# Kernel optimization log

Measured on AMD Instinct MI355X. Metric: run time of the kernel, lower is better.

## Reference

```python
import jax, jax.numpy as jnp
import numpy as np

T, G, L_UH, NZ = 512, 4096, 15, 1e-5

PHY_NAMES = ['ddf_min','ddf_plus','Kcum','Kf','exp_fe','Tbf','Ccum','SWI','Tbm','fcmin','fcmin_plus','vadose_max_level','hmets_alpha','vic_beta','hbv_beta','quickflow_k','quickflow_n','mmax','lamb','baseflow_k','baseflow_n','ET_efficiency','coef_vadose2phreatic','coef_phreatic']
BOUNDS = {'ddf_min':(0.,20.),'ddf_plus':(0.,20.),'Kcum':(.01,.2),'Kf':(0.,5.),'exp_fe':(0.,1.),'Tbf':(-5.,2.),'Ccum':(.005,.05),'SWI':(0.,.4),'Tbm':(-2.,3.),'fcmin':(0.,.1),'fcmin_plus':(.01,.25),'vadose_max_level':(.001,500.),'hmets_alpha':(0.,1.),'vic_beta':(.1,3.),'hbv_beta':(.5,3.),'quickflow_k':(-5.,-2.),'quickflow_n':(.5,2.),'mmax':(0.,100.),'lamb':(5.,10.),'baseflow_k':(-5.,-1.),'baseflow_n':(.5,2.),'ET_efficiency':(0.,3.),'coef_vadose2phreatic':(1e-5,.02),'coef_phreatic':(1e-5,.01)}

def setup_inputs():
    key = jax.random.key(0)
    k1, k2, k3, k4 = jax.random.split(key, 4)
    prcp = jax.random.uniform(k1, (T, G)) * 20.0   # mm/day
    tmean = jax.random.uniform(k2, (T, G)) * 40.0 - 15.0  # deg C, mixed rain/snow
    pet = jax.random.uniform(k3, (T, G)) * 6.0
    x = jnp.stack([prcp, tmean, pet], axis=-1).astype(jnp.float32)
    parameters = jax.random.normal(k4, (T, G, 39), dtype=jnp.float32)
    return {'x': x, 'parameters': parameters}

def _descale(v, lo, hi):
    return lo + v * (hi - lo)

def _unpack(parameters):
    # static params: last time step (dynamic_params=[], dy_drop=0 -> staPar path)
    last = parameters[-1, :, :35]
    p = {n: _descale(jax.nn.sigmoid(last[:, i]), *BOUNDS[n]) for i, n in enumerate(PHY_NAMES)}
    # blend weights: softmax within each weights_group (bounds [0,1] -> identity descale)
    for (s, e) in [(24, 27), (27, 30), (30, 33), (33, 35)]:
        w = jax.nn.softmax(last[:, s:e], axis=1)
        for j in range(e - s):
            p['w%d' % (s - 24 + j + 1)] = w[:, j]
    rp = jax.nn.sigmoid(parameters[-1, :, 35:39])
    r = {'alpha1': _descale(rp[:, 0], 0.3, 20.0), 'beta1': _descale(rp[:, 1], 0.01, 5.0),
         'alpha2': _descale(rp[:, 2], 0.5, 13.0), 'beta2': _descale(rp[:, 3], 0.15, 1.5)}
    return p, r

def _gamma_uh(a, b):
    # gamma-shaped unit hydrograph, normalized over L_UH steps, per grid cell
    t = jnp.arange(L_UH, dtype=jnp.float32) + 0.5
    w = t[None, :] ** (a[:, None] - 1.0) * jnp.exp(-t[None, :] / b[:, None])
    return w / jnp.sum(w, axis=1, keepdims=True)

def _route(q, uh):
    # causal depthwise convolution along time: out[t] = sum_k uh[k] * q[t-k]
    Tq = q.shape[0]
    qpad = jnp.pad(q, ((L_UH - 1, 0), (0, 0)))
    out = jnp.zeros_like(q)
    for k in range(L_UH):
        out = out + uh[None, :, k] * jax.lax.dynamic_slice_in_dim(qpad, L_UH - 1 - k, Tq, axis=0)
    return out

def _forward(x, parameters):
    p, r = _unpack(parameters)
    g = x.shape[1]
    vmax = p['vadose_max_level']
    relu = lambda v: jnp.maximum(v, 0.0)

    def snobal_hbv(tm, sf, rf, cm, sp, lw):
        ddf = jnp.minimum(p['ddf_min'] + p['ddf_plus'], p['ddf_min'] * (1.0 + p['Kcum'] * cm))
        pm = relu(ddf * (tm - p['Tbm']))
        rfz = jnp.minimum(p['Kf'] * jnp.maximum(p['Tbf'] - tm, NZ), lw)
        sp = sp + sf + rfz
        melt = jnp.minimum(pm, sp + sf + rfz)
        cm = (cm + melt) * (sp > NZ).astype(sp.dtype)
        sp = jnp.maximum(sp - melt, NZ)
        wret = p['SWI'] * sp
        wtmp = lw + melt + rf
        ovf = relu(wtmp - wret)
        lw = jnp.where(ovf > 0, wret, wtmp)
        return sp, lw, cm, ovf

    def snobal_hmets(tm, sf, rf, cm, sp, lw):
        ddf = jnp.minimum(p['ddf_min'] + p['ddf_plus'], p['ddf_min'] * (1.0 + p['Kcum'] * cm))
        pm = relu(ddf * (tm - p['Tbm']))
        pfz = p['Kf'] * jnp.maximum(p['Tbf'] - tm, NZ) ** p['exp_fe']
        rfz = jnp.minimum(pfz, lw)
        lw = lw - rfz
        sp = sp + rfz
        melt = jnp.minimum(pm, sp + sf)
        sp = sp + sf - melt
        cm = (cm + melt) * (sp > NZ).astype(sp.dtype)
        wrf = jnp.maximum((p['fcmin'] + p['fcmin_plus']) * (1.0 - p['Ccum'] * cm), p['fcmin'])
        wret = wrf * sp
        wtmp = lw + melt + rf
        ovf = relu(wtmp - wret)
        lw = jnp.where(ovf > 0, wret, wtmp)
        cm = (cm + melt) * (sp > NZ).astype(sp.dtype)
        return sp, lw, cm, ovf

    def snobal_simple(tm, sf, rf, cm, sp):
        ddf = jnp.minimum(p['ddf_min'] + p['ddf_plus'], p['ddf_min'] * (1.0 + p['Kcum'] * cm))
        pm = relu(ddf * (tm - p['Tbm']))
        melt = jnp.minimum(pm, sp)
        sp = sp + sf - melt
        ovf = melt + rf
        cm = (cm + melt) * (sp > NZ).astype(sp.dtype)
        return sp, cm, ovf

    def step(state, xt):
        sp1, lw1, cm1, sp2, lw2, cm2, sp3, cm3, vad, phr = state
        prcp, tm, pet = xt[:, 0], xt[:, 1], xt[:, 2]
        rain = jnp.where(tm > 0.0, prcp, 0.0)
        snow = prcp - rain
        sp1, lw1, cm1, o1 = snobal_hbv(tm, snow, rain, cm1, sp1, lw1)
        sp2, lw2, cm2, o2 = snobal_hmets(tm, snow, rain, cm2, sp2, lw2)
        sp3, cm3, o3 = snobal_simple(tm, snow, rain, cm3, sp3)
        rr = p['w1'] * o1 + p['w2'] * o2 + p['w3'] * o3
        sprop = jnp.clip(vad / vmax, NZ, 1.0 - NZ)
        inf = (p['w4'] * rr * (1.0 - sprop) ** p['hbv_beta']
               + p['w5'] * rr * (1.0 - p['hmets_alpha'] * vad / vmax)
               + p['w6'] * rr * (1.0 - (1.0 - sprop) ** p['vic_beta']))
        inf = jnp.clip(inf, 0.0, rr)
        surface = rr - inf
        vad = vad + inf
        sprop = jnp.clip(vad / vmax, NZ, 1.0 - NZ)
        et = jnp.minimum(pet * p['ET_efficiency'] * sprop, vad)
        vad = vad - et
        qf_lin = 10.0 ** p['quickflow_k'] * vad
        qf_top = jnp.minimum(p['mmax'] * (vmax / p['quickflow_n']) / p['lamb'] ** p['quickflow_n'] * sprop ** p['quickflow_n'], vad)
        qf_vic = jnp.minimum(p['mmax'] * sprop ** p['quickflow_n'], vad)
        qf = jnp.minimum(p['w7'] * qf_lin + p['w8'] * qf_top + p['w9'] * qf_vic, vad)
        vad = vad - qf
        perc = p['coef_vadose2phreatic'] * vad
        vad = vad - perc
        phr = phr + perc
        bf = jnp.minimum(p['w10'] * 10.0 ** p['baseflow_k'] * phr
                         + p['w11'] * 10.0 ** p['baseflow_k'] * jnp.maximum(phr, NZ) ** p['baseflow_n'], phr)
        phr = phr - bf
        return (sp1, lw1, cm1, sp2, lw2, cm2, sp3, cm3, vad, phr), (surface + qf, bf)

    z = jnp.zeros((g,), dtype=x.dtype)
    init = (z,) * 10
    _, (quick, base) = jax.lax.scan(step, init, x)
    flow = _route(quick, _gamma_uh(r['alpha1'], r['beta1'])) + _route(base, _gamma_uh(r['alpha2'], r['beta2']))
    return flow  # [T, G]

def reference(x, parameters):
    return _forward(x, parameters)
```

## Files before the change

kernel.cpp:

```cpp
#include <hip/hip_runtime.h>

#define T_STEPS 512
#define G_CELLS 4096
#define L_UHN   15
#define GRP     8
#define NGRP    (T_STEPS / GRP)
#define CPB     64
#define NZF     1e-5f
#define LOG2E   1.44269504088896340736f
#define LOG2_10 3.32192809488736234787f

__device__ __forceinline__ float fexp2(float x) { return __builtin_amdgcn_exp2f(x); }
__device__ __forceinline__ float flog2(float x) { return __builtin_amdgcn_logf(x); }
__device__ __forceinline__ float fmed3(float x, float lo, float hi) { return __builtin_amdgcn_fmed3f(x, lo, hi); }
__device__ __forceinline__ float fpow(float a, float b) { return fexp2(b * flog2(a)); }
__device__ __forceinline__ float fexp(float x) { return fexp2(x * LOG2E); }
__device__ __forceinline__ float fsigmoid(float v) { return 1.0f / (1.0f + fexp(-v)); }
__device__ __forceinline__ float fdescale(float s, float lo, float hi) { return lo + s * (hi - lo); }

__device__ __forceinline__ void block_barrier() {
    asm volatile("s_waitcnt lgkmcnt(0)" ::: "memory");
    __builtin_amdgcn_s_barrier();
}


__device__ __forceinline__ void snow02_wave(const float* __restrict__ x,
                                            const float* __restrict__ pp,
                                            float (*ob)[2][GRP][CPB],
                                            int lane, int g)
{
    const float ddf_min  = fdescale(fsigmoid(pp[0]), 0.0f, 20.0f);
    const float ddf_plus = fdescale(fsigmoid(pp[1]), 0.0f, 20.0f);
    const float Kcum     = fdescale(fsigmoid(pp[2]), 0.01f, 0.2f);
    const float Kf       = fdescale(fsigmoid(pp[3]), 0.0f, 5.0f);
    const float Tbf      = fdescale(fsigmoid(pp[5]), -5.0f, 2.0f);
    const float SWI      = fdescale(fsigmoid(pp[7]), 0.0f, 0.4f);
    const float Tbm      = fdescale(fsigmoid(pp[8]), -2.0f, 3.0f);
    const float ddfsum   = ddf_min + ddf_plus;
    const float ddfK     = ddf_min * Kcum;

    float w0, w2_;
    {
        float r0 = pp[24], r1 = pp[25], r2 = pp[26];
        float m = fmaxf(fmaxf(r0, r1), r2);
        float e0 = fexp(r0 - m), e1 = fexp(r1 - m), e2 = fexp(r2 - m);
        float inv = 1.0f / (e0 + e1 + e2);
        w0 = e0 * inv; w2_ = e2 * inv;
    }

    float sp0 = 0.f, lw0 = 0.f, cm0 = 0.f;
    float sp2 = 0.f, cm2 = 0.f;

    float bR[GRP], bS[GRP], bD[GRP], bX[GRP];
    float rawP[GRP], rawT[GRP];
    #pragma unroll
    for (int j = 0; j < GRP; ++j) {
        size_t a = ((size_t)j * G_CELLS + (size_t)g) * 3;
        rawP[j] = x[a]; rawT[j] = x[a + 1];
    }
    #pragma unroll
    for (int j = 0; j < GRP; ++j) {
        float tm = rawT[j], prcp = rawP[j];
        bR[j] = (tm > 0.0f) ? prcp : 0.0f;
        bS[j] = prcp - bR[j];
        bD[j] = tm - Tbm;
        bX[j] = Kf * fmaxf(Tbf - tm, NZF);
    }

    for (int k = 0; k <= NGRP + 5; ++k) {
        block_barrier();
        if (k < NGRP) {
            const int kn = (k + 1 < NGRP) ? k + 1 : NGRP - 1;
            #pragma unroll
            for (int j = 0; j < GRP; ++j) {
                size_t a = ((size_t)(kn * GRP + j) * G_CELLS + (size_t)g) * 3;
                rawP[j] = x[a]; rawT[j] = x[a + 1];
            }

            const int b = k & 1;
            #pragma unroll
            for (int j = 0; j < GRP; ++j) {
                const float rain = bR[j], snow = bS[j], dtm = bD[j];
                float oA, oB;
                {
                    float ddf  = fminf(ddfsum, fmaf(ddfK, cm0, ddf_min));
                    float pm   = fmaxf(ddf * dtm, 0.0f);
                    float rfz  = fminf(bX[j], lw0);
                    sp0 = sp0 + snow + rfz;
                    float melt = fminf(pm, sp0 + snow + rfz);
                    cm0 = (sp0 > NZF) ? (cm0 + melt) : 0.0f;
                    sp0 = fmaxf(sp0 - melt, NZF);
                    float wret = SWI * sp0;
                    float wtmp = lw0 + melt + rain;
                    oA = fmaxf(wtmp - wret, 0.0f);
                    lw0 = fminf(wtmp, wret);
                }
                {
                    float ddf  = fminf(ddfsum, fmaf(ddfK, cm2, ddf_min));
                    float pm   = fmaxf(ddf * dtm, 0.0f);
                    float melt = fminf(pm, sp2);
                    sp2 = sp2 + snow - melt;
                    oB = melt + rain;
                    cm2 = (sp2 > NZF) ? (cm2 + melt) : 0.0f;
                }
                ob[b][0][j][lane] = w0 * oA + w2_ * oB;
            }

            #pragma unroll
            for (int j = 0; j < GRP; ++j) {
                float tm = rawT[j], prcp = rawP[j];
                bR[j] = (tm > 0.0f) ? prcp : 0.0f;
                bS[j] = prcp - bR[j];
                bD[j] = tm - Tbm;
                bX[j] = Kf * fmaxf(Tbf - tm, NZF);
            }
        }
    }
}

__device__ __forceinline__ void snow1_wave(const float* __restrict__ x,
                                           const float* __restrict__ pp,
                                           float (*ob)[2][GRP][CPB],
                                           int lane, int g)
{
    const float ddf_min  = fdescale(fsigmoid(pp[0]), 0.0f, 20.0f);
    const float ddf_plus = fdescale(fsigmoid(pp[1]), 0.0f, 20.0f);
    const float Kcum     = fdescale(fsigmoid(pp[2]), 0.01f, 0.2f);
    const float Kf       = fdescale(fsigmoid(pp[3]), 0.0f, 5.0f);
    const float exp_fe   = fdescale(fsigmoid(pp[4]), 0.0f, 1.0f);
    const float Tbf      = fdescale(fsigmoid(pp[5]), -5.0f, 2.0f);
    const float Ccum     = fdescale(fsigmoid(pp[6]), 0.005f, 0.05f);
    const float Tbm      = fdescale(fsigmoid(pp[8]), -2.0f, 3.0f);
    const float fcmin    = fdescale(fsigmoid(pp[9]), 0.0f, 0.1f);
    const float fcsum    = fcmin + fdescale(fsigmoid(pp[10]), 0.01f, 0.25f);
    const float ddfsum   = ddf_min + ddf_plus;
    const float ddfK     = ddf_min * Kcum;

    float w1;
    {
        float r0 = pp[24], r1 = pp[25], r2 = pp[26];
        float m = fmaxf(fmaxf(r0, r1), r2);
        float e0 = fexp(r0 - m), e1 = fexp(r1 - m), e2 = fexp(r2 - m);
        w1 = e1 / (e0 + e1 + e2);
    }

    float sp = 0.f, lw = 0.f, cm = 0.f;

    float bR[GRP], bS[GRP], bD[GRP], bX[GRP];
    float rawP[GRP], rawT[GRP];
    #pragma unroll
    for (int j = 0; j < GRP; ++j) {
        size_t a = ((size_t)j * G_CELLS + (size_t)g) * 3;
        rawP[j] = x[a]; rawT[j] = x[a + 1];
    }
    #pragma unroll
    for (int j = 0; j < GRP; ++j) {
        float tm = rawT[j], prcp = rawP[j];
        bR[j] = (tm > 0.0f) ? prcp : 0.0f;
        bS[j] = prcp - bR[j];
        bD[j] = tm - Tbm;
        bX[j] = Kf * fpow(fmaxf(Tbf - tm, NZF), exp_fe);
    }

    for (int k = 0; k <= NGRP + 5; ++k) {
        block_barrier();
        if (k < NGRP) {
            const int kn = (k + 1 < NGRP) ? k + 1 : NGRP - 1;
            #pragma unroll
            for (int j = 0; j < GRP; ++j) {
                size_t a = ((size_t)(kn * GRP + j) * G_CELLS + (size_t)g) * 3;
                rawP[j] = x[a]; rawT[j] = x[a + 1];
            }

            const int b = k & 1;
            #pragma unroll
            for (int j = 0; j < GRP; ++j) {
                const float rain = bR[j], snow = bS[j], dtm = bD[j];
                float ddf  = fminf(ddfsum, fmaf(ddfK, cm, ddf_min));
                float pm   = fmaxf(ddf * dtm, 0.0f);
                float rfz  = fminf(bX[j], lw);
                lw -= rfz; sp += rfz;
                float melt = fminf(pm, sp + snow);
                sp = sp + snow - melt;
                cm = (sp > NZF) ? (cm + melt) : 0.0f;
                float wrf  = fmaxf(fcsum * (1.0f - Ccum * cm), fcmin);
                float wret = wrf * sp;
                float wtmp = lw + melt + rain;
                float o    = fmaxf(wtmp - wret, 0.0f);
                lw = fminf(wtmp, wret);
                cm = (sp > NZF) ? (cm + melt) : 0.0f;
                ob[b][1][j][lane] = w1 * o;
            }

            #pragma unroll
            for (int j = 0; j < GRP; ++j) {
                float tm = rawT[j], prcp = rawP[j];
                bR[j] = (tm > 0.0f) ? prcp : 0.0f;
                bS[j] = prcp - bR[j];
                bD[j] = tm - Tbm;
                bX[j] = Kf * fpow(fmaxf(Tbf - tm, NZF), exp_fe);
            }
        }
    }
}

__device__ __forceinline__ void vad_wave(const float* __restrict__ x,
                                         const float* __restrict__ pp,
                                         float (*ob)[2][GRP][CPB],
                                         float (*pr)[2][GRP][CPB],
                                         int lane, int g)
{
    const float vmax        = fdescale(fsigmoid(pp[11]), 0.001f, 500.0f);
    const float hmets_alpha = fdescale(fsigmoid(pp[12]), 0.0f, 1.0f);
    const float vic_beta    = fdescale(fsigmoid(pp[13]), 0.1f, 3.0f);
    const float hbv_beta    = fdescale(fsigmoid(pp[14]), 0.5f, 3.0f);
    const float quickflow_k = fdescale(fsigmoid(pp[15]), -5.0f, -2.0f);
    const float qn          = fdescale(fsigmoid(pp[16]), 0.5f, 2.0f);
    const float mmax        = fdescale(fsigmoid(pp[17]), 0.0f, 100.0f);
    const float lamb        = fdescale(fsigmoid(pp[18]), 5.0f, 10.0f);
    const float ET_eff      = fdescale(fsigmoid(pp[21]), 0.0f, 3.0f);
    const float cv2p        = fdescale(fsigmoid(pp[22]), 1e-5f, 0.02f);

    float w4, w5, w6, w7, w8, w9;
    {
        float r0 = pp[27], r1 = pp[28], r2 = pp[29];
        float m = fmaxf(fmaxf(r0, r1), r2);
        float e0 = fexp(r0 - m), e1 = fexp(r1 - m), e2 = fexp(r2 - m);
        float inv = 1.0f / (e0 + e1 + e2);
        w4 = e0 * inv; w5 = e1 * inv; w6 = e2 * inv;
    }
    {
        float r0 = pp[30], r1 = pp[31], r2 = pp[32];
        float m = fmaxf(fmaxf(r0, r1), r2);
        float e0 = fexp(r0 - m), e1 = fexp(r1 - m), e2 = fexp(r2 - m);
        float inv = 1.0f / (e0 + e1 + e2);
        w7 = e0 * inv; w8 = e1 * inv; w9 = e2 * inv;
    }

    const float inv_vmax    = 1.0f / vmax;
    const float qk10        = fexp2(quickflow_k * LOG2_10);
    const float qf_top_coef = mmax * (vmax / qn) * fexp2(-qn * flog2(lamb));
    const float w7qk        = w7 * qk10;
    const float hi_clamp    = 1.0f - NZF;

    float vad = 0.f;

    float rrCur[GRP], rrNext[GRP];
    float pe[GRP], rawPrev[GRP], rawNew[GRP];

    for (int k = 0; k <= NGRP + 5; ++k) {
        block_barrier();

        if (k < NGRP) {
            #pragma unroll
            for (int j = 0; j < GRP; ++j)
                rawNew[j] = x[((size_t)(k * GRP + j) * G_CELLS + (size_t)g) * 3 + 2];
        }

        if (k - 1 >= 0 && k - 1 < NGRP) {
            const int b = (k - 1) & 1;
            #pragma unroll
            for (int j = 0; j < GRP; ++j)
                rrNext[j] = ob[b][0][j][lane] + ob[b][1][j][lane];
        }

        if (k - 2 >= 0 && k - 2 < NGRP) {
            const int kg = k - 2;
            const int slot = kg & 3;
            #pragma unroll
            for (int j = 0; j < GRP; ++j) {
                const float rrj = rrCur[j];
                float vv = vad * inv_vmax;
                float sprop = fmed3(vv, NZF, hi_clamp);
                float l1 = flog2(1.0f - sprop);
                float phbv = fexp2(hbv_beta * l1);
                float pvic = fexp2(vic_beta * l1);
                float a4 = w4 * rrj;
                float a6 = w6 * rrj;
                float base = w5 * rrj * (1.0f - hmets_alpha * vv) + a6;
                float inf = fmaf(a4, phbv, fmaf(-a6, pvic, base));
                inf = fmed3(inf, 0.0f, rrj);
                float surface = rrj - inf;
                vad += inf;
                vv = vad * inv_vmax;
                float sprop1 = fmed3(vv, NZF, hi_clamp);
                float lq = flog2(sprop1);
                float et = fminf(pe[j] * sprop1, vad);
                vad -= et;
                float spq    = fexp2(qn * lq);
                float qf_top = fminf(qf_top_coef * spq, vad);
                float qf_vic = fminf(mmax * spq, vad);
                float qf = fminf(fmaf(w7qk, vad, fmaf(w8, qf_top, w9 * qf_vic)), vad);
                vad -= qf;
                float perc = cv2p * vad;
                vad -= perc;

                pr[slot][0][j][lane] = perc;
                pr[slot][1][j][lane] = surface + qf;
            }
        }

        #pragma unroll
        for (int j = 0; j < GRP; ++j) rrCur[j] = rrNext[j];
        #pragma unroll
        for (int j = 0; j < GRP; ++j) pe[j] = rawPrev[j] * ET_eff;
        #pragma unroll
        for (int j = 0; j < GRP; ++j) rawPrev[j] = rawNew[j];
    }
}

__device__ __forceinline__ void phr_wave(const float* __restrict__ pp,
                                         float (*pr)[2][GRP][CPB],
                                         float (*bfr)[GRP][CPB],
                                         int lane)
{
    const float baseflow_k = fdescale(fsigmoid(pp[19]), -5.0f, -1.0f);
    const float bn         = fdescale(fsigmoid(pp[20]), 0.5f, 2.0f);
    float w10, w11;
    {
        float r0 = pp[33], r1 = pp[34];
        float m = fmaxf(r0, r1);
        float e0 = fexp(r0 - m), e1 = fexp(r1 - m);
        float inv = 1.0f / (e0 + e1);
        w10 = e0 * inv; w11 = e1 * inv;
    }
    const float bk10 = fexp2(baseflow_k * LOG2_10);
    const float c_b1 = w10 * bk10, c_b2 = w11 * bk10;

    float phr = 0.f;
    float pcCur[GRP], pcNext[GRP];

    for (int k = 0; k <= NGRP + 5; ++k) {
        block_barrier();

        if (k - 3 >= 0 && k - 3 < NGRP) {
            const int slot = (k - 3) & 3;
            #pragma unroll
            for (int j = 0; j < GRP; ++j) pcNext[j] = pr[slot][0][j][lane];
        }

        if (k - 4 >= 0 && k - 4 < NGRP) {
            const int kg = k - 4;
            const int bslot = kg & 1;
            #pragma unroll
            for (int j = 0; j < GRP; ++j) {
                phr += pcCur[j];
                float pb = fexp2(bn * flog2(fmaxf(phr, NZF)));
                float bf = fminf(fmaf(c_b1, phr, c_b2 * pb), phr);
                phr -= bf;
                bfr[bslot][j][lane] = bf;
            }
        }

        #pragma unroll
        for (int j = 0; j < GRP; ++j) pcCur[j] = pcNext[j];
    }
}

__device__ __forceinline__ void route_wave(const float* __restrict__ pp,
                                           float (*pr)[2][GRP][CPB],
                                           float (*bfr)[GRP][CPB],
                                           float* __restrict__ out,
                                           int lane, int g)
{
    const float a1 = fdescale(fsigmoid(pp[35]), 0.3f, 20.0f);
    const float b1 = fdescale(fsigmoid(pp[36]), 0.01f, 5.0f);
    const float a2 = fdescale(fsigmoid(pp[37]), 0.5f, 13.0f);
    const float b2 = fdescale(fsigmoid(pp[38]), 0.15f, 1.5f);

    const float LOG2T[L_UHN] = {
        -1.0f, 0.58496250072116f, 1.32192809488736f, 1.80735492205760f,
        2.16992500144231f, 2.45943161863730f, 2.70043971814109f,
        2.90689059560852f, 3.08746284125034f, 3.24792751344359f,
        3.39231742277876f, 3.52356195605701f, 3.64385618977472f,
        3.75488750216347f, 3.85798099512757f };

    float uh1[L_UHN], uh2[L_UHN];
    {
        float rb1 = LOG2E / b1, rb2 = LOG2E / b2;
        float s1 = 0.0f, s2 = 0.0f;
        #pragma unroll
        for (int kk = 0; kk < L_UHN; ++kk) {
            float tk = (float)kk + 0.5f;
            float v1 = fexp2((a1 - 1.0f) * LOG2T[kk] - tk * rb1);
            float v2 = fexp2((a2 - 1.0f) * LOG2T[kk] - tk * rb2);
            uh1[kk] = v1; uh2[kk] = v2; s1 += v1; s2 += v2;
        }
        float i1 = 1.0f / s1, i2 = 1.0f / s2;
        #pragma unroll
        for (int kk = 0; kk < L_UHN; ++kk) { uh1[kk] *= i1; uh2[kk] *= i2; }
    }

    float fut[L_UHN];
    #pragma unroll
    for (int kk = 0; kk < L_UHN; ++kk) fut[kk] = 0.0f;

    float qCur[GRP], bCur[GRP], qNext[GRP], bNext[GRP];

    for (int k = 0; k <= NGRP + 5; ++k) {
        block_barrier();

        if (k - 5 >= 0 && k - 5 < NGRP) {
            const int s4  = (k - 5) & 3;
            const int s2_ = (k - 5) & 1;
            #pragma unroll
            for (int j = 0; j < GRP; ++j) {
                qNext[j] = pr[s4][1][j][lane];
                bNext[j] = bfr[s2_][j][lane];
            }
        }

        if (k - 6 >= 0 && k - 6 < NGRP) {
            const int kg = k - 6;
            #pragma unroll
            for (int j = 0; j < GRP; ++j) {
                const float qt = qCur[j];
                const float bf = bCur[j];
                #pragma unroll
                for (int kk = 0; kk < L_UHN; ++kk)
                    fut[kk] = fmaf(uh1[kk], qt, fmaf(uh2[kk], bf, fut[kk]));
                out[(size_t)(kg * GRP + j) * G_CELLS + (size_t)g] = fut[0];
                #pragma unroll
                for (int kk = 0; kk < L_UHN - 1; ++kk) fut[kk] = fut[kk + 1];
                fut[L_UHN - 1] = 0.0f;
            }
        }

        #pragma unroll
        for (int j = 0; j < GRP; ++j) { qCur[j] = qNext[j]; bCur[j] = bNext[j]; }
    }
}

__global__ __launch_bounds__(320, 1) void pipeline_kernel(
    const float* __restrict__ x, const float* __restrict__ params,
    float* __restrict__ out)
{
    __shared__ float ob[2][2][GRP][CPB];
    __shared__ float pr[4][2][GRP][CPB];
    __shared__ float bfr[2][GRP][CPB];
    const int lane = threadIdx.x & 63;
    const int wave = threadIdx.x >> 6;
    const int g    = blockIdx.x * CPB + lane;
    const float* pp = params + ((size_t)(T_STEPS - 1) * G_CELLS + (size_t)g) * 39;

    if (wave == 0)      phr_wave(pp, pr, bfr, lane);
    else if (wave == 1) snow02_wave(x, pp, ob, lane, g);
    else if (wave == 2) snow1_wave(x, pp, ob, lane, g);
    else if (wave == 3) vad_wave(x, pp, ob, pr, lane, g);
    else                route_wave(pp, pr, bfr, out, lane, g);
}

extern "C" void kernel_launch(void* const* d_in, const int* in_sizes, int n_in,
                              void* d_out, int out_size, void* d_ws, size_t ws_size,
                              hipStream_t stream) {
    const float* x      = (const float*)d_in[0];
    const float* params = (const float*)d_in[1];
    float* out          = (float*)d_out;
    pipeline_kernel<<<dim3(G_CELLS / CPB), dim3(320), 0, stream>>>(x, params, out);
}
```

Measured before the change: 71.12 us.

## Merge phreatic and routing waves, double group size, streamline vadose step

Folds the phreatic-store wave into the routing wave, so the block drops from five specialized waves to four and the bfr shared buffer and one pipeline stage go away. The time-step group size doubles, halving the number of barrier-separated pipeline iterations. The vadose recurrence is also reworked: the top/vic quickflow power terms use precomputed log2 offsets, the vad update is expressed via fma, and percolation becomes a single multiply. The merged wave now carries both the phreatic recurrence and the 15-tap convolution on its critical path, and the larger group raises register pressure.

```diff
diff --git a/kernel.cpp b/kernel.cpp
--- a/kernel.cpp
+++ b/kernel.cpp
@@ -3,7 +3,7 @@
 #define T_STEPS 512
 #define G_CELLS 4096
 #define L_UHN   15
-#define GRP     8
+#define GRP     16
 #define NGRP    (T_STEPS / GRP)
 #define CPB     64
 #define NZF     1e-5f
@@ -67,7 +67,7 @@
         bX[j] = Kf * fmaxf(Tbf - tm, NZF);
     }
 
-    for (int k = 0; k <= NGRP + 5; ++k) {
+    for (int k = 0; k <= NGRP + 3; ++k) {
         block_barrier();
         if (k < NGRP) {
             const int kn = (k + 1 < NGRP) ? k + 1 : NGRP - 1;
@@ -162,7 +162,7 @@
         bX[j] = Kf * fpow(fmaxf(Tbf - tm, NZF), exp_fe);
     }
 
-    for (int k = 0; k <= NGRP + 5; ++k) {
+    for (int k = 0; k <= NGRP + 3; ++k) {
         block_barrier();
         if (k < NGRP) {
             const int kn = (k + 1 < NGRP) ? k + 1 : NGRP - 1;
@@ -242,13 +242,16 @@
     const float qf_top_coef = mmax * (vmax / qn) * fexp2(-qn * flog2(lamb));
     const float w7qk        = w7 * qk10;
     const float hi_clamp    = 1.0f - NZF;
+    const float l2top       = flog2(qf_top_coef);
+    const float l2vic       = flog2(mmax);
+    const float one_m_cv2p  = 1.0f - cv2p;
 
     float vad = 0.f;
 
     float rrCur[GRP], rrNext[GRP];
     float pe[GRP], rawPrev[GRP], rawNew[GRP];
 
-    for (int k = 0; k <= NGRP + 5; ++k) {
+    for (int k = 0; k <= NGRP + 3; ++k) {
         block_barrier();
 
         if (k < NGRP) {
@@ -270,30 +273,31 @@
             #pragma unroll
             for (int j = 0; j < GRP; ++j) {
                 const float rrj = rrCur[j];
-                float vv = vad * inv_vmax;
-                float sprop = fmed3(vv, NZF, hi_clamp);
-                float l1 = flog2(1.0f - sprop);
+                float vv0 = vad * inv_vmax;
+                float om  = fmed3(1.0f - vv0, NZF, hi_clamp);
+                float l1  = flog2(om);
                 float phbv = fexp2(hbv_beta * l1);
                 float pvic = fexp2(vic_beta * l1);
                 float a4 = w4 * rrj;
                 float a6 = w6 * rrj;
-                float base = w5 * rrj * (1.0f - hmets_alpha * vv) + a6;
+                float base = fmaf(w5 * rrj, fmaf(-hmets_alpha, vv0, 1.0f), a6);
                 float inf = fmaf(a4, phbv, fmaf(-a6, pvic, base));
                 inf = fmed3(inf, 0.0f, rrj);
                 float surface = rrj - inf;
-                vad += inf;
-                vv = vad * inv_vmax;
-                float sprop1 = fmed3(vv, NZF, hi_clamp);
+                float vad1 = vad + inf;
+                float vv1  = fmaf(inf, inv_vmax, vv0);
+                float sprop1 = fmed3(vv1, NZF, hi_clamp);
                 float lq = flog2(sprop1);
-                float et = fminf(pe[j] * sprop1, vad);
-                vad -= et;
-                float spq    = fexp2(qn * lq);
-                float qf_top = fminf(qf_top_coef * spq, vad);
-                float qf_vic = fminf(mmax * spq, vad);
-                float qf = fminf(fmaf(w7qk, vad, fmaf(w8, qf_top, w9 * qf_vic)), vad);
-                vad -= qf;
-                float perc = cv2p * vad;
-                vad -= perc;
+                float topt = fexp2(fmaf(qn, lq, l2top));
+                float vict = fexp2(fmaf(qn, lq, l2vic));
+                float vad2 = fmaxf(fmaf(-pe[j], sprop1, vad1), 0.0f);
+                float qf_top = fminf(topt, vad2);
+                float qf_vic = fminf(vict, vad2);
+                float S  = fmaf(w7qk, vad2, fmaf(w8, qf_top, w9 * qf_vic));
+                float qf = fminf(S, vad2);
+                float vad3 = vad2 - qf;
+                float perc = cv2p * vad3;
+                vad = vad3 * one_m_cv2p;
 
                 pr[slot][0][j][lane] = perc;
                 pr[slot][1][j][lane] = surface + qf;
@@ -309,10 +313,10 @@
     }
 }
 
-__device__ __forceinline__ void phr_wave(const float* __restrict__ pp,
-                                         float (*pr)[2][GRP][CPB],
-                                         float (*bfr)[GRP][CPB],
-                                         int lane)
+__device__ __forceinline__ void phr_route_wave(const float* __restrict__ pp,
+                                               float (*pr)[2][GRP][CPB],
+                                               float* __restrict__ out,
+                                               int lane, int g)
 {
     const float baseflow_k = fdescale(fsigmoid(pp[19]), -5.0f, -1.0f);
     const float bn         = fdescale(fsigmoid(pp[20]), 0.5f, 2.0f);
@@ -327,42 +331,6 @@
     const float bk10 = fexp2(baseflow_k * LOG2_10);
     const float c_b1 = w10 * bk10, c_b2 = w11 * bk10;
 
-    float phr = 0.f;
-    float pcCur[GRP], pcNext[GRP];
-
-    for (int k = 0; k <= NGRP + 5; ++k) {
-        block_barrier();
-
-        if (k - 3 >= 0 && k - 3 < NGRP) {
-            const int slot = (k - 3) & 3;
-            #pragma unroll
-            for (int j = 0; j < GRP; ++j) pcNext[j] = pr[slot][0][j][lane];
-        }
-
-        if (k - 4 >= 0 && k - 4 < NGRP) {
-            const int kg = k - 4;
-            const int bslot = kg & 1;
-            #pragma unroll
-            for (int j = 0; j < GRP; ++j) {
-                phr += pcCur[j];
-                float pb = fexp2(bn * flog2(fmaxf(phr, NZF)));
-                float bf = fminf(fmaf(c_b1, phr, c_b2 * pb), phr);
-                phr -= bf;
-                bfr[bslot][j][lane] = bf;
-            }
-        }
-
-        #pragma unroll
-        for (int j = 0; j < GRP; ++j) pcCur[j] = pcNext[j];
-    }
-}
-
-__device__ __forceinline__ void route_wave(const float* __restrict__ pp,
-                                           float (*pr)[2][GRP][CPB],
-                                           float (*bfr)[GRP][CPB],
-                                           float* __restrict__ out,
-                                           int lane, int g)
-{
     const float a1 = fdescale(fsigmoid(pp[35]), 0.3f, 20.0f);
     const float b1 = fdescale(fsigmoid(pp[36]), 0.01f, 5.0f);
     const float a2 = fdescale(fsigmoid(pp[37]), 0.5f, 13.0f);
@@ -391,31 +359,35 @@
         for (int kk = 0; kk < L_UHN; ++kk) { uh1[kk] *= i1; uh2[kk] *= i2; }
     }
 
+    float phr = 0.f;
     float fut[L_UHN];
     #pragma unroll
     for (int kk = 0; kk < L_UHN; ++kk) fut[kk] = 0.0f;
 
-    float qCur[GRP], bCur[GRP], qNext[GRP], bNext[GRP];
-
-    for (int k = 0; k <= NGRP + 5; ++k) {
+    float pcCur[GRP], qCur[GRP], pcNext[GRP], qNext[GRP];
+
+    for (int k = 0; k <= NGRP + 3; ++k) {
         block_barrier();
 
-        if (k - 5 >= 0 && k - 5 < NGRP) {
-            const int s4  = (k - 5) & 3;
-            const int s2_ = (k - 5) & 1;
-            #pragma unroll
-            for (int j = 0; j < GRP; ++j) {
-                qNext[j] = pr[s4][1][j][lane];
-                bNext[j] = bfr[s2_][j][lane];
-            }
-        }
-
-        if (k - 6 >= 0 && k - 6 < NGRP) {
-            const int kg = k - 6;
-            #pragma unroll
-            for (int j = 0; j < GRP; ++j) {
+        if (k - 3 >= 0 && k - 3 < NGRP) {
+            const int slot = (k - 3) & 3;
+            #pragma unroll
+            for (int j = 0; j < GRP; ++j) {
+                pcNext[j] = pr[slot][0][j][lane];
+                qNext[j]  = pr[slot][1][j][lane];
+            }
+        }
+
+        if (k - 4 >= 0 && k - 4 < NGRP) {
+            const int kg = k - 4;
+            #pragma unroll
+            for (int j = 0; j < GRP; ++j) {
+                phr += pcCur[j];
+                float pb = fexp2(bn * flog2(fmaxf(phr, NZF)));
+                float bf = fminf(fmaf(c_b1, phr, c_b2 * pb), phr);
+                phr -= bf;
+
                 const float qt = qCur[j];
-                const float bf = bCur[j];
                 #pragma unroll
                 for (int kk = 0; kk < L_UHN; ++kk)
                     fut[kk] = fmaf(uh1[kk], qt, fmaf(uh2[kk], bf, fut[kk]));
@@ -427,27 +399,25 @@
         }
 
         #pragma unroll
-        for (int j = 0; j < GRP; ++j) { qCur[j] = qNext[j]; bCur[j] = bNext[j]; }
-    }
-}
-
-__global__ __launch_bounds__(320, 1) void pipeline_kernel(
+        for (int j = 0; j < GRP; ++j) { pcCur[j] = pcNext[j]; qCur[j] = qNext[j]; }
+    }
+}
+
+__global__ __launch_bounds__(256, 1) void pipeline_kernel(
     const float* __restrict__ x, const float* __restrict__ params,
     float* __restrict__ out)
 {
     __shared__ float ob[2][2][GRP][CPB];
     __shared__ float pr[4][2][GRP][CPB];
-    __shared__ float bfr[2][GRP][CPB];
     const int lane = threadIdx.x & 63;
     const int wave = threadIdx.x >> 6;
     const int g    = blockIdx.x * CPB + lane;
     const float* pp = params + ((size_t)(T_STEPS - 1) * G_CELLS + (size_t)g) * 39;
 
-    if (wave == 0)      phr_wave(pp, pr, bfr, lane);
-    else if (wave == 1) snow02_wave(x, pp, ob, lane, g);
-    else if (wave == 2) snow1_wave(x, pp, ob, lane, g);
-    else if (wave == 3) vad_wave(x, pp, ob, pr, lane, g);
-    else                route_wave(pp, pr, bfr, out, lane, g);
+    if (wave == 0)      snow02_wave(x, pp, ob, lane, g);
+    else if (wave == 1) snow1_wave(x, pp, ob, lane, g);
+    else if (wave == 2) vad_wave(x, pp, ob, pr, lane, g);
+    else                phr_route_wave(pp, pr, out, lane, g);
 }
 
 extern "C" void kernel_launch(void* const* d_in, const int* in_sizes, int n_in,
@@ -456,5 +426,5 @@
     const float* x      = (const float*)d_in[0];
     const float* params = (const float*)d_in[1];
     float* out          = (float*)d_out;
-    pipeline_kernel<<<dim3(G_CELLS / CPB), dim3(320), 0, stream>>>(x, params, out);
-}
+    pipeline_kernel<<<dim3(G_CELLS / CPB), dim3(256), 0, stream>>>(x, params, out);
+}
```

Measured after the change: 69.44 us. -2.4%, faster.
